# Kernel tuning notes

Hardware: AMD Instinct MI355X
Metric: run time of the kernel (lower is better)

Reference implementation:

```python
import jax, jax.numpy as jnp
from jax import lax
import numpy as np

N, T, D, H = 256, 64, 1024, 1024


def setup_inputs() -> dict:
    key = jax.random.key(0)
    ks = jax.random.split(key, 6)
    x = jax.random.normal(ks[0], (N, T, D), dtype=jnp.float32)
    A = jax.random.normal(ks[1], (N, H, 4, 4), dtype=jnp.float32)
    Wx = jax.random.normal(ks[2], (D, 4 * H), dtype=jnp.float32) / np.sqrt(D)
    Wh = jax.random.normal(ks[3], (H, 4 * H), dtype=jnp.float32) / np.sqrt(H)
    Wattn = jax.random.normal(ks[4], (H, 4 * H), dtype=jnp.float32) / np.sqrt(H)
    b = jnp.zeros((4 * H,), dtype=jnp.float32)
    return {"x": x, "A": A, "Wx": Wx, "Wh": Wh, "Wattn": Wattn, "b": b}


def reference(x, A, Wx, Wh, Wattn, b):
    n, t, d = x.shape
    h_dim = A.shape[1]
    A_flat = A.reshape(n, h_dim, 16)           # (N, H, 16) keys/values
    h0 = jnp.mean(A_flat, axis=-1)             # mean over 4x4 grid
    scale = 1.0 / (h_dim ** 0.5)

    def step(carry, xt):
        h, c = carry
        # scaled dot-product attention over 16 spatial positions
        scores = jnp.einsum('nh,nhp->np', h, A_flat) * scale
        w = jax.nn.softmax(scores, axis=1)      # (N, 16)
        attn = jnp.einsum('nhp,np->nh', A_flat, w)
        # fused LSTM gate preactivations
        a = xt @ Wx + h @ Wh + attn @ Wattn + b  # (N, 4H)
        i, f, o, g = jnp.split(a, 4, axis=1)
        c_next = jax.nn.sigmoid(f) * c + jax.nn.sigmoid(i) * jnp.tanh(g)
        h_next = jax.nn.sigmoid(o) * jnp.tanh(c_next)
        return (h_next, c_next), h_next

    xs = jnp.swapaxes(x, 0, 1)                  # (T, N, D)
    _, hs = lax.scan(step, (h0, h0), xs)
    return jnp.swapaxes(hs, 0, 1)               # (N, T, H)
```

## Files before the change

kernel.cpp:

```cpp
#include <hip/hip_runtime.h>
#include <cstdint>
#include <cstddef>

#define T_S 64

typedef __attribute__((ext_vector_type(4))) float f32x4;
typedef __attribute__((ext_vector_type(2))) float f32x2;
typedef __attribute__((ext_vector_type(8))) short bh8;

__device__ __forceinline__ unsigned short f2b(float f) {
  uint32_t x = __builtin_bit_cast(uint32_t, f);
  uint32_t r = (x + 0x7FFFu + ((x >> 16) & 1u)) >> 16;
  return (unsigned short)r;
}
__device__ __forceinline__ float b2f(unsigned short u) {
  uint32_t v = ((uint32_t)u) << 16;
  return __builtin_bit_cast(float, v);
}

__device__ __forceinline__ unsigned ld_u32_l3(const void* p) {
  unsigned r;
  asm volatile("global_load_dword %0, %1, off sc0 sc1\n\ts_waitcnt vmcnt(0)"
               : "=v"(r) : "v"(p) : "memory");
  return r;
}
__device__ __forceinline__ void st_u32_l3(void* p, unsigned v) {
  asm volatile("global_store_dword %0, %1, off sc0 sc1" :: "v"(p), "v"(v) : "memory");
}

__device__ __forceinline__ void gbar(int* bar, int target) {
  __syncthreads();
  if (threadIdx.x == 0) {
    int one = 1;
    asm volatile("s_waitcnt vmcnt(0)\n\t"
                 "global_atomic_add %0, %1, off sc1"
                 :: "v"(bar), "v"(one) : "memory");
    int v;
    do {
      __builtin_amdgcn_s_sleep(1);
      asm volatile("global_load_dword %0, %1, off sc0 sc1\n\ts_waitcnt vmcnt(0)"
                   : "=v"(v) : "v"(bar) : "memory");
    } while (v < target);
  }
  __syncthreads();
}


__global__ void k_conv(const float* __restrict__ src, unsigned short* __restrict__ dst, int n4) {
  int i = blockIdx.x * blockDim.x + threadIdx.x;
  int stride = gridDim.x * blockDim.x;
  for (; i < n4; i += stride) {
    float4 v = ((const float4*)src)[i];
    ushort4 o; o.x = f2b(v.x); o.y = f2b(v.y); o.z = f2b(v.z); o.w = f2b(v.w);
    ((ushort4*)dst)[i] = o;
  }
}

__global__ __launch_bounds__(256) void k_tw3(
    const float* __restrict__ Wx, const float* __restrict__ Wh,
    const float* __restrict__ Wa,
    unsigned short* __restrict__ WxT, unsigned short* __restrict__ PW) {
  __shared__ float tile[64][65];
  int j0 = blockIdx.x * 64;
  int k0 = blockIdx.y * 64;
  int z = blockIdx.z;
  const float* src = (z == 0) ? Wx : (z == 1) ? Wh : Wa;
  for (int i = threadIdx.x; i < 4096; i += 256) {
    int r = i >> 6, c = i & 63;
    tile[r][c] = src[(size_t)(k0 + r) * 4096 + (j0 + c)];
  }
  __syncthreads();
  for (int i = threadIdx.x; i < 4096; i += 256) {
    int r = i >> 6, c = i & 63;
    int col = j0 + r;
    unsigned short v = f2b(tile[c][r]);
    if (z == 0) {
      WxT[(size_t)col * 1024 + (k0 + c)] = v;
    } else {
      int q = col >> 10, hcol = col & 1023;
      int prow = (hcol >> 5) * 128 + q * 32 + (hcol & 31);
      PW[(size_t)prow * 2048 + (size_t)(z - 1) * 1024 + (k0 + c)] = v;
    }
  }
}

__global__ __launch_bounds__(256) void k_conv_x2(
    const float* __restrict__ x, unsigned short* __restrict__ xb2) {
  int b = blockIdx.x, tid = threadIdx.x;
  #pragma unroll
  for (int rr = 0; rr < 4; ++rr) {
    int r = b * 4 + rr;
    int t = r >> 8, n = r & 255;
    const float4* src = (const float4*)(x + ((size_t)n * 64 + t) * 1024);
    float4 v = src[tid];
    ushort4 o; o.x = f2b(v.x); o.y = f2b(v.y); o.z = f2b(v.z); o.w = f2b(v.w);
    ((ushort4*)(xb2 + (size_t)r * 1024))[tid] = o;
  }
}

__global__ __launch_bounds__(256) void k_init2(
    const float* __restrict__ A, unsigned short* __restrict__ hx,
    float* __restrict__ cst) {
  int idx = blockIdx.x * 256 + threadIdx.x;
  const float4* a4 = (const float4*)(A + (size_t)idx * 16);
  float s = 0.f;
  #pragma unroll
  for (int q = 0; q < 4; ++q) { float4 v = a4[q]; s += v.x + v.y + v.z + v.w; }
  s *= 0.0625f;
  cst[idx] = s;
  hx[(size_t)(idx >> 10) * 2048 + (idx & 1023)] = f2b(s);
}

__global__ __launch_bounds__(256) void k_init1(
    const float* __restrict__ A, unsigned short* __restrict__ hb,
    float* __restrict__ cst) {
  int idx = blockIdx.x * 256 + threadIdx.x;
  const float4* a4 = (const float4*)(A + (size_t)idx * 16);
  float s = 0.f;
  #pragma unroll
  for (int q = 0; q < 4; ++q) { float4 v = a4[q]; s += v.x + v.y + v.z + v.w; }
  s *= 0.0625f;
  cst[idx] = s;
  hb[idx] = f2b(s);
}

template <int PERM>
__global__ __launch_bounds__(512) void k_gemm_t(
    const unsigned short* __restrict__ Asrc,
    const unsigned short* __restrict__ Bt,
    unsigned short* __restrict__ C) {
  __shared__ __align__(16) unsigned short smem[36864];
  int tid = threadIdx.x;
  int bx = blockIdx.x, by = blockIdx.y;
  int lane = tid & 63, wave = tid >> 6;
  int wr = wave >> 1, wc = wave & 1;
  int srow = tid >> 3;
  int scol = (tid & 7) * 8;
  const unsigned short* arow0 = Asrc + ((size_t)(bx * 128 + srow)) * 1024 + scol;
  const unsigned short* arow1 = arow0 + (size_t)64 * 1024;
  const unsigned short* brow0 = Bt + ((size_t)(by * 128 + srow)) * 1024 + scol;
  const unsigned short* brow1 = brow0 + (size_t)64 * 1024;

  f32x4 acc[2][4];
  #pragma unroll
  for (int m = 0; m < 2; ++m)
    #pragma unroll
    for (int nn = 0; nn < 4; ++nn) acc[m][nn] = {0.f, 0.f, 0.f, 0.f};

  uint4 ra0, ra1, rb0, rb1;
  auto gload = [&](int kt) {
    int k0 = kt * 64;
    ra0 = *(const uint4*)(arow0 + k0);
    ra1 = *(const uint4*)(arow1 + k0);
    rb0 = *(const uint4*)(brow0 + k0);
    rb1 = *(const uint4*)(brow1 + k0);
  };
  int frow = lane & 15, fk = (lane >> 4) * 8;
  gload(0);
  int cur = 0;
  for (int kt = 0; kt < 16; ++kt) {
    unsigned short* As = smem + cur * 18432;
    unsigned short* Bs = As + 9216;
    *(uint4*)(As + srow * 72 + scol) = ra0;
    *(uint4*)(As + (srow + 64) * 72 + scol) = ra1;
    *(uint4*)(Bs + srow * 72 + scol) = rb0;
    *(uint4*)(Bs + (srow + 64) * 72 + scol) = rb1;
    __syncthreads();
    if (kt + 1 < 16) gload(kt + 1);
    #pragma unroll
    for (int kk = 0; kk < 2; ++kk) {
      bh8 af[2], bf[4];
      #pragma unroll
      for (int m = 0; m < 2; ++m)
        af[m] = *(const bh8*)(As + (wr * 32 + m * 16 + frow) * 72 + kk * 32 + fk);
      #pragma unroll
      for (int nn = 0; nn < 4; ++nn)
        bf[nn] = *(const bh8*)(Bs + (wc * 64 + nn * 16 + frow) * 72 + kk * 32 + fk);
      #pragma unroll
      for (int m = 0; m < 2; ++m)
        #pragma unroll
        for (int nn = 0; nn < 4; ++nn)
          acc[m][nn] = __builtin_amdgcn_mfma_f32_16x16x32_bf16(af[m], bf[nn], acc[m][nn], 0, 0, 0);
    }
    cur ^= 1;
  }
  int rbase = bx * 128 + wr * 32 + (lane >> 4) * 4;
  int cbase = by * 128 + wc * 64 + frow;
  #pragma unroll
  for (int m = 0; m < 2; ++m)
    #pragma unroll
    for (int nn = 0; nn < 4; ++nn)
      #pragma unroll
      for (int reg = 0; reg < 4; ++reg) {
        size_t row = rbase + m * 16 + reg;
        int c = cbase + nn * 16;
        int q = c >> 10, hcol = c & 1023;
        size_t off = PERM ? ((size_t)row * 4096 + (hcol >> 5) * 128 + q * 32 + (hcol & 31))
                          : ((size_t)row * 4096 + c);
        C[off] = f2b(acc[m][nn][reg]);
      }
}

__global__ __launch_bounds__(512, 1) void k_steps(
    const unsigned short* __restrict__ Ab,
    const unsigned short* __restrict__ PW,
    const unsigned short* __restrict__ xprojP,
    const float* __restrict__ bias,
    unsigned short* __restrict__ hxA,
    unsigned short* __restrict__ hxB,
    const float* __restrict__ cst0,
    float* __restrict__ out,
    int* __restrict__ bars) {
  extern __shared__ __align__(16) char sm[];
  const int tid = threadIdx.x;
  const int bid = blockIdx.x;
  const int lane = tid & 63, wave = tid >> 6;
  const int wm = wave & 1, wc = wave >> 1;
  const int frow = lane & 15, fg = lane >> 4;
  const int g = bid >> 5, j = bid & 31;
  const int nbase = g * 32;
  const int nA = nbase + j;
  int* mybar = bars + (g << 6);

  const int erow = tid >> 4;
  const int el2 = (tid & 15) * 2;
  const int hcol = j * 32 + el2;

  float creg[2];
  float brg[4][2];
  {
    const float* cp = cst0 + (size_t)(nbase + erow) * 1024 + hcol;
    creg[0] = cp[0]; creg[1] = cp[1];
    #pragma unroll
    for (int q = 0; q < 4; ++q) {
      brg[q][0] = bias[q * 1024 + hcol];
      brg[q][1] = bias[q * 1024 + hcol + 1];
    }
  }

  const int c16 = (tid & 15) * 16;
  const char* bB0 = (const char*)(PW + (size_t)(j * 128 + erow) * 2048) + c16;
  const char* bB1 = bB0 + 32 * 4096;
  const char* bB2 = bB0 + 64 * 4096;
  const char* bB3 = bB0 + 96 * 4096;
  const char* aBA = (const char*)(hxA + (size_t)(nbase + erow) * 2048) + c16;
  const char* aBB = (const char*)(hxB + (size_t)(nbase + erow) * 2048) + c16;

  const int wA = (erow * 256 + c16) ^ ((erow & 7) << 4);
  const int qA = ((wm * 16 + frow) * 256 + fg * 16) ^ ((frow & 7) << 4);
  const int qB = ((wc * 32 + frow) * 256 + fg * 16) ^ ((frow & 7) << 4);

  uint4 sa0, sa1, sa2, sa3;
  uint4 sb00, sb01, sb02, sb03;
  uint4 sb10, sb11, sb12, sb13;
  uint4 sb20, sb21, sb22, sb23;
  uint4 sb30, sb31, sb32, sb33;

#define LOADST(st, ktL) \
  asm volatile("global_load_dwordx4 %0, %1, off offset:%c2 sc0 sc1" : "=v"(sa##st) : "v"(aB), "i"((ktL) * 256)); \
  asm volatile("global_load_dwordx4 %0, %1, off offset:%c2" : "=v"(sb##st##0) : "v"(bB0), "i"((ktL) * 256)); \
  asm volatile("global_load_dwordx4 %0, %1, off offset:%c2" : "=v"(sb##st##1) : "v"(bB1), "i"((ktL) * 256)); \
  asm volatile("global_load_dwordx4 %0, %1, off offset:%c2" : "=v"(sb##st##2) : "v"(bB2), "i"((ktL) * 256)); \
  asm volatile("global_load_dwordx4 %0, %1, off offset:%c2" : "=v"(sb##st##3) : "v"(bB3), "i"((ktL) * 256));

#define GSTEP(kt, st, bufo, WN) { \
  asm volatile("s_waitcnt vmcnt(" #WN ")" ::: "memory"); \
  *(uint4*)(sm + (bufo) + wA) = sa##st; \
  *(uint4*)(sm + (bufo) + 8192 + wA) = sb##st##0; \
  *(uint4*)(sm + (bufo) + 8192 + wA + 8192) = sb##st##1; \
  *(uint4*)(sm + (bufo) + 8192 + wA + 16384) = sb##st##2; \
  *(uint4*)(sm + (bufo) + 8192 + wA + 24576) = sb##st##3; \
  if ((kt) + 4 < 16) { LOADST(st, (kt) + 4) } \
  asm volatile("s_waitcnt lgkmcnt(0)" ::: "memory"); \
  __builtin_amdgcn_s_barrier(); \
  _Pragma("unroll") \
  for (int kk = 0; kk < 4; ++kk) { \
    bh8 af  = *(const bh8*)(sm + (bufo) + (qA ^ (kk << 6))); \
    bh8 bf0 = *(const bh8*)(sm + (bufo) + 8192 + (qB ^ (kk << 6))); \
    bh8 bf1 = *(const bh8*)(sm + (bufo) + 8192 + 4096 + (qB ^ (kk << 6))); \
    acc0 = __builtin_amdgcn_mfma_f32_16x16x32_bf16(af, bf0, acc0, 0, 0, 0); \
    acc1 = __builtin_amdgcn_mfma_f32_16x16x32_bf16(af, bf1, acc1, 0, 0, 0); \
  } \
}

  int nb = 0;
  for (int t = 0; t < 64; ++t) {
    unsigned short* hxc = (t & 1) ? hxB : hxA;
    unsigned short* hxn = (t & 1) ? hxA : hxB;
    const char* aB = (t & 1) ? aBB : aBA;

    {
      unsigned hh = ld_u32_l3(hxc + (size_t)nA * 2048 + tid * 2);
      float hv0 = b2f((unsigned short)(hh & 0xffff));
      float hv1 = b2f((unsigned short)(hh >> 16));
      const unsigned short* ap = Ab + (size_t)nA * 16384 + tid * 32;
      bh8 a0 = *(const bh8*)(ap);
      bh8 a1 = *(const bh8*)(ap + 8);
      bh8 a2 = *(const bh8*)(ap + 16);
      bh8 a3 = *(const bh8*)(ap + 24);
      float s[16];
      #pragma unroll
      for (int p = 0; p < 8; ++p) {
        s[p]     = hv0 * b2f((unsigned short)a0[p]) + hv1 * b2f((unsigned short)a2[p]);
        s[8 + p] = hv0 * b2f((unsigned short)a1[p]) + hv1 * b2f((unsigned short)a3[p]);
      }
      #pragma unroll
      for (int p = 0; p < 16; ++p) {
        float v = s[p];
        #pragma unroll
        for (int off = 32; off > 0; off >>= 1) v += __shfl_xor(v, off);
        s[p] = v;
      }
      float* red = (float*)sm;
      float* scs = red + 128;
      if (lane == 0) {
        #pragma unroll
        for (int p = 0; p < 16; ++p) red[wave * 16 + p] = s[p];
      }
      __syncthreads();
      if (tid < 16) {
        float v = 0.f;
        #pragma unroll
        for (int wv = 0; wv < 8; ++wv) v += red[wv * 16 + tid];
        scs[tid] = v * 0.03125f;
      }
      __syncthreads();
      float sc[16];
      #pragma unroll
      for (int p = 0; p < 16; ++p) sc[p] = scs[p];
      float m = sc[0];
      #pragma unroll
      for (int p = 1; p < 16; ++p) m = fmaxf(m, sc[p]);
      float w[16]; float sum = 0.f;
      #pragma unroll
      for (int p = 0; p < 16; ++p) { w[p] = __expf(sc[p] - m); sum += w[p]; }
      float inv = 1.0f / sum;
      float at0 = 0.f, at1 = 0.f;
      #pragma unroll
      for (int p = 0; p < 8; ++p) {
        at0 += w[p] * b2f((unsigned short)a0[p]) + w[8 + p] * b2f((unsigned short)a1[p]);
        at1 += w[p] * b2f((unsigned short)a2[p]) + w[8 + p] * b2f((unsigned short)a3[p]);
      }
      at0 *= inv; at1 *= inv;
      unsigned packed = (unsigned)f2b(at0) | ((unsigned)f2b(at1) << 16);
      st_u32_l3(hxc + (size_t)nA * 2048 + 1024 + tid * 2, packed);
    }
    nb += 1; gbar(mybar, nb * 32);

    {
      uint4 xq = *(const uint4*)(xprojP + ((size_t)(t * 256 + nbase + erow)) * 4096
                                 + j * 128 + (tid & 15) * 8);
      f32x4 acc0 = {0.f, 0.f, 0.f, 0.f};
      f32x4 acc1 = {0.f, 0.f, 0.f, 0.f};
      LOADST(0, 0) LOADST(1, 1) LOADST(2, 2) LOADST(3, 3)
      GSTEP(0, 0, 0, 15)      GSTEP(1, 1, 40960, 15)
      GSTEP(2, 2, 0, 15)      GSTEP(3, 3, 40960, 15)
      GSTEP(4, 0, 0, 15)      GSTEP(5, 1, 40960, 15)
      GSTEP(6, 2, 0, 15)      GSTEP(7, 3, 40960, 15)
      GSTEP(8, 0, 0, 15)      GSTEP(9, 1, 40960, 15)
      GSTEP(10, 2, 0, 15)     GSTEP(11, 3, 40960, 15)
      GSTEP(12, 0, 0, 15)     GSTEP(13, 1, 40960, 10)
      GSTEP(14, 2, 0, 5)      GSTEP(15, 3, 40960, 0)
      __syncthreads();
      float* a_lds = (float*)sm;
      unsigned short* xp = (unsigned short*)(sm + 16896);
      {
        int r0 = wm * 16 + fg * 4;
        int c0 = wc * 32 + frow;
        #pragma unroll
        for (int r = 0; r < 4; ++r) {
          a_lds[(r0 + r) * 132 + c0]      = acc0[r];
          a_lds[(r0 + r) * 132 + c0 + 16] = acc1[r];
        }
        *(uint4*)(xp + erow * 136 + (tid & 15) * 8) = xq;
      }
      __syncthreads();
      {
        float h2[2];
        #pragma unroll
        for (int e = 0; e < 2; ++e) {
          float pre[4];
          #pragma unroll
          for (int q = 0; q < 4; ++q)
            pre[q] = a_lds[erow * 132 + q * 32 + el2 + e]
                   + b2f(xp[erow * 136 + q * 32 + el2 + e]) + brg[q][e];
          float si = 1.0f / (1.0f + __expf(-pre[0]));
          float sf = 1.0f / (1.0f + __expf(-pre[1]));
          float so = 1.0f / (1.0f + __expf(-pre[2]));
          float tg = 2.0f / (1.0f + __expf(-2.0f * pre[3])) - 1.0f;
          float cn = sf * creg[e] + si * tg;
          creg[e] = cn;
          h2[e] = so * (2.0f / (1.0f + __expf(-2.0f * cn)) - 1.0f);
        }
        f32x2 o2 = {h2[0], h2[1]};
        __builtin_nontemporal_store(o2,
            (f32x2*)(out + ((size_t)(nbase + erow) * T_S + t) * 1024 + hcol));
        unsigned hp = (unsigned)f2b(h2[0]) | ((unsigned)f2b(h2[1]) << 16);
        st_u32_l3(hxn + (size_t)(nbase + erow) * 2048 + hcol, hp);
      }
    }
    nb += 1; gbar(mybar, nb * 32);
  }
#undef GSTEP
#undef LOADST
}


__global__ __launch_bounds__(256) void k_prep_w(
    const float* __restrict__ Wx, const float* __restrict__ Wh,
    const float* __restrict__ Wa, unsigned short* __restrict__ WT) {
  __shared__ float tile[64][65];
  int j0 = blockIdx.x * 64;
  int k0 = blockIdx.y * 64;
  const float* src; int kk0;
  if (k0 < 1024)      { src = Wx; kk0 = k0; }
  else if (k0 < 2048) { src = Wh; kk0 = k0 - 1024; }
  else                { src = Wa; kk0 = k0 - 2048; }
  for (int i = threadIdx.x; i < 4096; i += 256) {
    int r = i >> 6, c = i & 63;
    tile[r][c] = src[(size_t)(kk0 + r) * 4096 + (j0 + c)];
  }
  __syncthreads();
  for (int i = threadIdx.x; i < 4096; i += 256) {
    int r = i >> 6, c = i & 63;
    WT[(size_t)(j0 + r) * 3072 + (k0 + c)] = f2b(tile[c][r]);
  }
}

__global__ __launch_bounds__(256) void k_attn(
    const float* __restrict__ A, const unsigned short* __restrict__ hb,
    unsigned short* __restrict__ attnb) {
  int n = blockIdx.x;
  int tid = threadIdx.x;
  int lane = tid & 63, wave = tid >> 6;
  float areg[4][16];
  float s[16];
  #pragma unroll
  for (int p = 0; p < 16; ++p) s[p] = 0.f;
  #pragma unroll
  for (int r = 0; r < 4; ++r) {
    int h = r * 256 + tid;
    size_t base = (size_t)n * 1024 + h;
    const float4* a4 = (const float4*)(A + base * 16);
    #pragma unroll
    for (int q = 0; q < 4; ++q) {
      float4 v = a4[q];
      areg[r][q*4+0] = v.x; areg[r][q*4+1] = v.y;
      areg[r][q*4+2] = v.z; areg[r][q*4+3] = v.w;
    }
    float hv = b2f(hb[base]);
    #pragma unroll
    for (int p = 0; p < 16; ++p) s[p] += hv * areg[r][p];
  }
  #pragma unroll
  for (int p = 0; p < 16; ++p) {
    float v = s[p];
    #pragma unroll
    for (int off = 32; off > 0; off >>= 1) v += __shfl_xor(v, off);
    s[p] = v;
  }
  __shared__ float red[4][16];
  __shared__ float sc_sh[16];
  if (lane == 0) {
    #pragma unroll
    for (int p = 0; p < 16; ++p) red[wave][p] = s[p];
  }
  __syncthreads();
  if (tid < 16) {
    sc_sh[tid] = (red[0][tid] + red[1][tid] + red[2][tid] + red[3][tid]) * 0.03125f;
  }
  __syncthreads();
  float sc[16];
  #pragma unroll
  for (int p = 0; p < 16; ++p) sc[p] = sc_sh[p];
  float m = sc[0];
  #pragma unroll
  for (int p = 1; p < 16; ++p) m = fmaxf(m, sc[p]);
  float e[16]; float sum = 0.f;
  #pragma unroll
  for (int p = 0; p < 16; ++p) { e[p] = __expf(sc[p] - m); sum += e[p]; }
  float inv = 1.0f / sum;
  #pragma unroll
  for (int r = 0; r < 4; ++r) {
    float a = 0.f;
    #pragma unroll
    for (int p = 0; p < 16; ++p) a += areg[r][p] * e[p];
    attnb[(size_t)n * 1024 + r * 256 + tid] = f2b(a * inv);
  }
}

__global__ __launch_bounds__(512) void k_step(
    const unsigned short* __restrict__ xb,
    const unsigned short* __restrict__ WT,
    const float* __restrict__ bias,
    const unsigned short* __restrict__ hr,
    const unsigned short* __restrict__ atb,
    unsigned short* __restrict__ hw,
    float* __restrict__ cst,
    float* __restrict__ out,
    int t)
{
  __shared__ __align__(16) unsigned short smem[18432];
  int tid = threadIdx.x;
  int bn = blockIdx.x;
  int bm = blockIdx.y;
  int lane = tid & 63;
  int wave = tid >> 6;
  int wr = wave >> 1;
  int wc = wave & 1;
  int nbase = bm * 64;
  int j0 = bn * 16;
  int srow = tid >> 3;
  int scol = (tid & 7) * 8;
  int bj = ((srow >> 4) * 1024) + j0 + (srow & 15);
  const unsigned short* bsrc = WT + (size_t)bj * 3072 + scol;
  f32x4 acc0 = {0.f, 0.f, 0.f, 0.f};
  f32x4 acc1 = {0.f, 0.f, 0.f, 0.f};
  uint4 ra, rb;
  auto gload = [&](int kt) {
    int k0 = kt * 64;
    const unsigned short* src; size_t rs; int kloc;
    if (k0 < 1024)      { src = xb + (size_t)t * 1024; rs = (size_t)T_S * 1024; kloc = k0; }
    else if (k0 < 2048) { src = hr;  rs = 1024; kloc = k0 - 1024; }
    else                { src = atb; rs = 1024; kloc = k0 - 2048; }
    ra = *(const uint4*)(src + (size_t)(nbase + srow) * rs + kloc + scol);
    rb = *(const uint4*)(bsrc + k0);
  };
  int frow = lane & 15;
  int fk = (lane >> 4) * 8;
  gload(0);
  int cur = 0;
  for (int kt = 0; kt < 48; ++kt) {
    unsigned short* As = smem + cur * 4608;
    unsigned short* Bs = smem + 9216 + cur * 4608;
    *(uint4*)(As + srow * 72 + scol) = ra;
    *(uint4*)(Bs + srow * 72 + scol) = rb;
    __syncthreads();
    if (kt + 1 < 48) gload(kt + 1);
    #pragma unroll
    for (int kk = 0; kk < 2; ++kk) {
      bh8 af  = *(const bh8*)(As + (wr * 16 + frow) * 72 + kk * 32 + fk);
      bh8 bf0 = *(const bh8*)(Bs + (wc * 32 + frow) * 72 + kk * 32 + fk);
      bh8 bf1 = *(const bh8*)(Bs + (wc * 32 + 16 + frow) * 72 + kk * 32 + fk);
      acc0 = __builtin_amdgcn_mfma_f32_16x16x32_bf16(af, bf0, acc0, 0, 0, 0);
      acc1 = __builtin_amdgcn_mfma_f32_16x16x32_bf16(af, bf1, acc1, 0, 0, 0);
    }
    cur ^= 1;
  }
  __syncthreads();
  float* a_lds = (float*)smem;
  {
    int r0 = wr * 16 + (lane >> 4) * 4;
    int c0 = wc * 32 + frow;
    #pragma unroll
    for (int reg = 0; reg < 4; ++reg) {
      a_lds[(r0 + reg) * 65 + c0]      = acc0[reg];
      a_lds[(r0 + reg) * 65 + c0 + 16] = acc1[reg];
    }
  }
  __syncthreads();
  #pragma unroll
  for (int r = 0; r < 2; ++r) {
    int pi = r * 512 + tid;
    int row = pi >> 4, gl = pi & 15;
    int n = nbase + row;
    int gcol = j0 + gl;
    float ii = a_lds[row * 65 + gl]      + bias[gcol];
    float ff = a_lds[row * 65 + 16 + gl] + bias[1024 + gcol];
    float oo = a_lds[row * 65 + 32 + gl] + bias[2048 + gcol];
    float gg = a_lds[row * 65 + 48 + gl] + bias[3072 + gcol];
    size_t ci = (size_t)n * 1024 + gcol;
    float cold = cst[ci];
    float si = 1.0f / (1.0f + __expf(-ii));
    float sf = 1.0f / (1.0f + __expf(-ff));
    float so = 1.0f / (1.0f + __expf(-oo));
    float tg = 2.0f / (1.0f + __expf(-2.0f * gg)) - 1.0f;
    float cn = sf * cold + si * tg;
    float hn = so * (2.0f / (1.0f + __expf(-2.0f * cn)) - 1.0f);
    cst[ci] = cn;
    out[((size_t)n * T_S + t) * 1024 + gcol] = hn;
    hw[ci] = f2b(hn);
  }
}


extern "C" void kernel_launch(void* const* d_in, const int* in_sizes, int n_in,
                              void* d_out, int out_size, void* d_ws, size_t ws_size,
                              hipStream_t stream) {
  const float* x  = (const float*)d_in[0];
  const float* A  = (const float*)d_in[1];
  const float* Wx = (const float*)d_in[2];
  const float* Wh = (const float*)d_in[3];
  const float* Wa = (const float*)d_in[4];
  const float* b  = (const float*)d_in[5];
  float* out = (float*)d_out;
  char* ws = (char*)d_ws;

  if (ws_size >= 204476416ull) {
    unsigned short* WxT   = (unsigned short*)(ws);
    unsigned short* PW    = (unsigned short*)(ws + 8388608);
    unsigned short* xb2   = (unsigned short*)(ws + 25165824);
    unsigned short* Ab    = (unsigned short*)(ws + 58720256);
    unsigned short* xprojP= (unsigned short*)(ws + 67108864);
    unsigned short* hxA   = (unsigned short*)(ws + 201326592);
    unsigned short* hxB   = (unsigned short*)(ws + 202375168);
    float* cst            = (float*)(ws + 203423744);
    int* bars             = (int*)(ws + 204472320);

    hipFuncSetAttribute((const void*)k_steps,
                        hipFuncAttributeMaxDynamicSharedMemorySize, 86016);

    k_tw3<<<dim3(64, 16, 3), 256, 0, stream>>>(Wx, Wh, Wa, WxT, PW);
    k_conv_x2<<<4096, 256, 0, stream>>>(x, xb2);
    k_conv<<<1024, 256, 0, stream>>>(A, Ab, 1048576);
    k_init2<<<1024, 256, 0, stream>>>(A, hxA, cst);
    k_gemm_t<1><<<dim3(128, 32), 512, 0, stream>>>(xb2, WxT, xprojP);
    hipMemsetAsync(bars, 0, 2048, stream);
    k_steps<<<256, 512, 86016, stream>>>(Ab, PW, xprojP, b, hxA, hxB, cst, out, bars);
  } else if (ws_size >= 61341696ull) {
    unsigned short* WT  = (unsigned short*)(ws);
    unsigned short* xb  = (unsigned short*)(ws + 25165824);
    unsigned short* hA  = (unsigned short*)(ws + 58720256);
    unsigned short* hB  = (unsigned short*)(ws + 59244544);
    unsigned short* atb = (unsigned short*)(ws + 59768832);
    float* cst          = (float*)(ws + 60293120);

    k_prep_w<<<dim3(64, 48), 256, 0, stream>>>(Wx, Wh, Wa, WT);
    k_conv<<<2048, 256, 0, stream>>>(x, xb, 4194304);
    k_init1<<<1024, 256, 0, stream>>>(A, hA, cst);
    for (int t = 0; t < 64; ++t) {
      const unsigned short* hr = (t & 1) ? hB : hA;
      unsigned short* hwv      = (t & 1) ? hA : hB;
      k_attn<<<256, 256, 0, stream>>>(A, hr, atb);
      k_step<<<dim3(64, 4), 512, 0, stream>>>(xb, WT, b, hr, atb, hwv, cst, out, t);
    }
  }
}
```

Measured before the change: 1.331 ms.

## Replace atomic counter barrier with per-block flag slots and overlap loads

The group barrier now has each block write its step count into its own slot, and 32 lanes poll all slots together, instead of atomically incrementing one shared counter. This removes atomic contention and serialization on a single address. The change also issues the h load alongside the A loads before a single wait, widens the LDS XOR swizzle from 8 to 16 rows, and loads xproj with a nontemporal hint. In exchange, polling traffic rises, and the slot memory must start zeroed and hold monotonic values.

```diff
diff --git a/kernel.cpp b/kernel.cpp
--- a/kernel.cpp
+++ b/kernel.cpp
@@ -18,29 +18,24 @@
   return __builtin_bit_cast(float, v);
 }
 
-__device__ __forceinline__ unsigned ld_u32_l3(const void* p) {
-  unsigned r;
-  asm volatile("global_load_dword %0, %1, off sc0 sc1\n\ts_waitcnt vmcnt(0)"
-               : "=v"(r) : "v"(p) : "memory");
-  return r;
-}
 __device__ __forceinline__ void st_u32_l3(void* p, unsigned v) {
   asm volatile("global_store_dword %0, %1, off sc0 sc1" :: "v"(p), "v"(v) : "memory");
 }
 
-__device__ __forceinline__ void gbar(int* bar, int target) {
-  __syncthreads();
-  if (threadIdx.x == 0) {
-    int one = 1;
-    asm volatile("s_waitcnt vmcnt(0)\n\t"
-                 "global_atomic_add %0, %1, off sc1"
-                 :: "v"(bar), "v"(one) : "memory");
+__device__ __forceinline__ void gbar(int* slots, int jslot, int target) {
+  __syncthreads();
+  int tid = threadIdx.x;
+  if (tid == 0)
+    asm volatile("global_store_dword %0, %1, off sc0 sc1"
+                 :: "v"(slots + jslot), "v"(target) : "memory");
+  if (tid < 64) {
+    const int* p = slots + (tid & 31);
     int v;
     do {
       __builtin_amdgcn_s_sleep(1);
       asm volatile("global_load_dword %0, %1, off sc0 sc1\n\ts_waitcnt vmcnt(0)"
-                   : "=v"(v) : "v"(bar) : "memory");
-    } while (v < target);
+                   : "=v"(v) : "v"(p) : "memory");
+    } while (__any(v < target));
   }
   __syncthreads();
 }
@@ -220,7 +215,7 @@
   const int g = bid >> 5, j = bid & 31;
   const int nbase = g * 32;
   const int nA = nbase + j;
-  int* mybar = bars + (g << 6);
+  int* myslots = bars + (g << 6);
 
   const int erow = tid >> 4;
   const int el2 = (tid & 15) * 2;
@@ -246,9 +241,9 @@
   const char* aBA = (const char*)(hxA + (size_t)(nbase + erow) * 2048) + c16;
   const char* aBB = (const char*)(hxB + (size_t)(nbase + erow) * 2048) + c16;
 
-  const int wA = (erow * 256 + c16) ^ ((erow & 7) << 4);
-  const int qA = ((wm * 16 + frow) * 256 + fg * 16) ^ ((frow & 7) << 4);
-  const int qB = ((wc * 32 + frow) * 256 + fg * 16) ^ ((frow & 7) << 4);
+  const int wA = (erow * 256 + c16) ^ ((erow & 15) << 4);
+  const int qA = ((wm * 16 + frow) * 256 + fg * 16) ^ ((frow & 15) << 4);
+  const int qB = ((wc * 32 + frow) * 256 + fg * 16) ^ ((frow & 15) << 4);
 
   uint4 sa0, sa1, sa2, sa3;
   uint4 sb00, sb01, sb02, sb03;
@@ -290,14 +285,18 @@
     const char* aB = (t & 1) ? aBB : aBA;
 
     {
-      unsigned hh = ld_u32_l3(hxc + (size_t)nA * 2048 + tid * 2);
-      float hv0 = b2f((unsigned short)(hh & 0xffff));
-      float hv1 = b2f((unsigned short)(hh >> 16));
+      unsigned hh;
+      asm volatile("global_load_dword %0, %1, off sc0 sc1"
+                   : "=v"(hh) : "v"(hxc + (size_t)nA * 2048 + tid * 2));
       const unsigned short* ap = Ab + (size_t)nA * 16384 + tid * 32;
       bh8 a0 = *(const bh8*)(ap);
       bh8 a1 = *(const bh8*)(ap + 8);
       bh8 a2 = *(const bh8*)(ap + 16);
       bh8 a3 = *(const bh8*)(ap + 24);
+      asm volatile("s_waitcnt vmcnt(0)" ::: "memory");
+      __builtin_amdgcn_sched_barrier(0);
+      float hv0 = b2f((unsigned short)(hh & 0xffff));
+      float hv1 = b2f((unsigned short)(hh >> 16));
       float s[16];
       #pragma unroll
       for (int p = 0; p < 8; ++p) {
@@ -345,11 +344,13 @@
       unsigned packed = (unsigned)f2b(at0) | ((unsigned)f2b(at1) << 16);
       st_u32_l3(hxc + (size_t)nA * 2048 + 1024 + tid * 2, packed);
     }
-    nb += 1; gbar(mybar, nb * 32);
+    nb += 1; gbar(myslots, j, nb);
 
     {
-      uint4 xq = *(const uint4*)(xprojP + ((size_t)(t * 256 + nbase + erow)) * 4096
-                                 + j * 128 + (tid & 15) * 8);
+      const unsigned short* xqp = xprojP + ((size_t)(t * 256 + nbase + erow)) * 4096
+                                  + j * 128 + (tid & 15) * 8;
+      uint4 xq;
+      asm volatile("global_load_dwordx4 %0, %1, off nt" : "=v"(xq) : "v"(xqp));
       f32x4 acc0 = {0.f, 0.f, 0.f, 0.f};
       f32x4 acc1 = {0.f, 0.f, 0.f, 0.f};
       LOADST(0, 0) LOADST(1, 1) LOADST(2, 2) LOADST(3, 3)
@@ -399,7 +400,7 @@
         st_u32_l3(hxn + (size_t)(nbase + erow) * 2048 + hcol, hp);
       }
     }
-    nb += 1; gbar(mybar, nb * 32);
+    nb += 1; gbar(myslots, j, nb);
   }
 #undef GSTEP
 #undef LOADST
```

After: 1.167 ms. 1.14x faster.
